# Performance work log

Measured on AMD Instinct MI355X. Metric: run time of the kernel, lower is better.

Reference implementation:

```python
import jax, jax.numpy as jnp
import numpy as np

HIDDEN = 512
IN_DIM = 512
N_ACT = 64
N_AGENTS = 8


def kalei_linear(x, ids, W, b, t):
    """x: [N, I]; ids: [N]; W: [O, I]; b: [O]; t: [A, O, I] -> [N, O].
    w_a = sign(W) * relu(|W| - sigmoid(t_a)); y_n = w_{ids[n]} @ x_n + b.
    """
    Wm = jnp.sign(W)[None] * jax.nn.relu(jnp.abs(W)[None] - jax.nn.sigmoid(t))  # [A,O,I]
    y = jnp.einsum('aoi,ni->nao', Wm, x)          # [N, A, O] batched masked GEMM
    y = jnp.take_along_axis(y, ids[:, None, None], axis=1)[:, 0]  # [N, O]
    return y + b[None, :]


def gru_cell(x, h, w_ih, w_hh, b_ih, b_hh):
    gi = x @ w_ih.T + b_ih
    gh = h @ w_hh.T + b_hh
    i_r, i_z, i_n = jnp.split(gi, 3, axis=-1)
    h_r, h_z, h_n = jnp.split(gh, 3, axis=-1)
    r = jax.nn.sigmoid(i_r + h_r)
    z = jax.nn.sigmoid(i_z + h_z)
    n = jnp.tanh(i_n + r * h_n)
    return (1.0 - z) * n + z * h


def setup_inputs() -> dict:
    key = jax.random.key(0)
    ks = jax.random.split(key, 20)
    B, A = 2048, N_AGENTS
    scale_init_lo, scale_init_hi = 3.0, 4.0  # -(rand*scale + bias) in [-4, -3]

    def thr(k, o, i):
        return -jax.random.uniform(k, (A, o, i), jnp.float32, scale_init_lo, scale_init_hi)

    w_scale = 0.05
    inp = {
        'inputs': jax.random.normal(ks[0], (B, A, IN_DIM), jnp.float32),
        'hidden_state': jax.random.normal(ks[1], (B, A, HIDDEN), jnp.float32),
        'agent_ids': jax.random.randint(ks[2], (B, A), 0, A),
        'fc1_w': jax.random.normal(ks[3], (HIDDEN, IN_DIM), jnp.float32) * w_scale,
        'fc1_b': jax.random.normal(ks[4], (HIDDEN,), jnp.float32) * w_scale,
        'fc1_t': thr(ks[5], HIDDEN, IN_DIM),
        'gru_wih': jax.random.normal(ks[6], (3 * HIDDEN, HIDDEN), jnp.float32) * w_scale,
        'gru_whh': jax.random.normal(ks[7], (3 * HIDDEN, HIDDEN), jnp.float32) * w_scale,
        'gru_bih': jax.random.normal(ks[8], (3 * HIDDEN,), jnp.float32) * w_scale,
        'gru_bhh': jax.random.normal(ks[9], (3 * HIDDEN,), jnp.float32) * w_scale,
        'fc2_w': jax.random.normal(ks[10], (HIDDEN, HIDDEN), jnp.float32) * w_scale,
        'fc2_b': jax.random.normal(ks[11], (HIDDEN,), jnp.float32) * w_scale,
        'fc2_t': thr(ks[12], HIDDEN, HIDDEN),
        'fc3_w': jax.random.normal(ks[13], (HIDDEN, HIDDEN), jnp.float32) * w_scale,
        'fc3_b': jax.random.normal(ks[14], (HIDDEN,), jnp.float32) * w_scale,
        'fc3_t': thr(ks[15], HIDDEN, HIDDEN),
        'fc4_w': jax.random.normal(ks[16], (N_ACT, HIDDEN), jnp.float32) * w_scale,
        'fc4_b': jax.random.normal(ks[17], (N_ACT,), jnp.float32) * w_scale,
        'fc4_t': thr(ks[18], N_ACT, HIDDEN),
    }
    return inp


def reference(inputs, hidden_state, agent_ids,
              fc1_w, fc1_b, fc1_t,
              gru_wih, gru_whh, gru_bih, gru_bhh,
              fc2_w, fc2_b, fc2_t,
              fc3_w, fc3_b, fc3_t,
              fc4_w, fc4_b, fc4_t):
    b, a, e = inputs.shape
    x = inputs.reshape(-1, e)                  # [N, e]
    ids = agent_ids.reshape(-1)                # [N]
    h_in = hidden_state.reshape(-1, HIDDEN)    # [N, H]

    x = jax.nn.relu(kalei_linear(x, ids, fc1_w, fc1_b, fc1_t))
    h = gru_cell(x, h_in, gru_wih, gru_whh, gru_bih, gru_bhh)
    q = jax.nn.relu(kalei_linear(h, ids, fc2_w, fc2_b, fc2_t))
    q = jax.nn.relu(kalei_linear(q, ids, fc3_w, fc3_b, fc3_t))
    q = kalei_linear(q, ids, fc4_w, fc4_b, fc4_t)
    return q.reshape(b, a, -1), h.reshape(b, a, -1)
```

## Files before the change

### kernel.cpp

```cpp
#include <hip/hip_runtime.h>
#include <hip/hip_bf16.h>
#include <stdint.h>

#define HID 512
#define NACT 64
#define NAG 8
#define NR 16384
#define BMT 128
#define MAXTILES 136

typedef __bf16 bf16_t;
typedef __bf16 bf16x4 __attribute__((ext_vector_type(4)));
typedef __bf16 bf16x8 __attribute__((ext_vector_type(8)));
typedef float  f32x16 __attribute__((ext_vector_type(16)));

#define MFMA32(a,b,c) __builtin_amdgcn_mfma_f32_32x32x16_bf16((a),(b),(c),0,0,0)

#define OFF_META 0
#define OFF_PERM 4096
#define OFF_WM1  (128*1024)
#define OFF_WM2  (OFF_WM1 + NAG*HID*HID*2)
#define OFF_WM3  (OFF_WM2 + NAG*HID*HID*2)
#define OFF_WM4  (OFF_WM3 + NAG*HID*HID*2)
#define OFF_WIH  (OFF_WM4 + NAG*NACT*HID*2)
#define OFF_WHH  (OFF_WIH + 3*HID*HID*2)
#define OFF_XS   (OFF_WHH + 3*HID*HID*2)
#define OFF_HS   (OFF_XS + (size_t)NR*HID*2)
#define OFF_B1   (OFF_HS + (size_t)NR*HID*2)

__device__ inline void load_lds16(const void* g, void* l) {
  __builtin_amdgcn_global_load_lds((__attribute__((address_space(1))) void*)g,
                                   (__attribute__((address_space(3))) void*)l,
                                   16, 0, 0);
}

template<int N> __device__ inline void wait_vmcnt() {
  asm volatile("s_waitcnt vmcnt(%0)" :: "n"(N) : "memory");
}
__device__ inline void wait_lgkm0() {
  asm volatile("s_waitcnt lgkmcnt(0)" ::: "memory");
}
#define BAR() __builtin_amdgcn_s_barrier()

__device__ inline bf16x8 lds_frag(const bf16_t* base, int r, int cb) {
  return *(const bf16x8*)((const char*)base + r*128 + ((cb*16) ^ ((r&7)<<4)));
}

__device__ inline void store8bf(void* dst, float4 a, float4 b) {
  union { bf16_t h[8]; uint4 u; } p;
  p.h[0]=(bf16_t)a.x; p.h[1]=(bf16_t)a.y; p.h[2]=(bf16_t)a.z; p.h[3]=(bf16_t)a.w;
  p.h[4]=(bf16_t)b.x; p.h[5]=(bf16_t)b.y; p.h[6]=(bf16_t)b.z; p.h[7]=(bf16_t)b.w;
  *(uint4*)dst = p.u;
}

__device__ inline float kmask(float w, float t) {
  float s = 1.f / (1.f + __expf(-t));
  float m = fabsf(w) - s;
  return m > 0.f ? copysignf(m, w) : 0.f;
}
__device__ inline float sigm(float x) { return 1.f / (1.f + __expf(-x)); }
__device__ inline float tanh_f(float x) {
  float e = __expf(2.f * fabsf(x));
  return copysignf(1.f - 2.f/(e + 1.f), x);
}

__global__ void k_prep(const float* __restrict__ f1w, const float* __restrict__ f1t,
                       const float* __restrict__ f2w, const float* __restrict__ f2t,
                       const float* __restrict__ f3w, const float* __restrict__ f3t,
                       const float* __restrict__ f4w, const float* __restrict__ f4t,
                       const float* __restrict__ gih, const float* __restrict__ ghh,
                       bf16_t* __restrict__ wm1, bf16_t* __restrict__ wm2,
                       bf16_t* __restrict__ wm3, bf16_t* __restrict__ wm4,
                       bf16_t* __restrict__ wihb, bf16_t* __restrict__ whhb,
                       int* __restrict__ meta)
{
  const int tid = threadIdx.x;
  if (blockIdx.x == 0 && tid < 32) meta[tid] = 0;
  long v = (long)blockIdx.x * 256 + tid;
  const long VR1 = 524288;
  if (v < 3*VR1) {
    int which = (int)(v / VR1);
    long e = (v - (long)which*VR1) * 4;
    const float* W = which==0 ? f1w : (which==1 ? f2w : f3w);
    const float* T = which==0 ? f1t : (which==1 ? f2t : f3t);
    bf16_t* O = which==0 ? wm1 : (which==1 ? wm2 : wm3);
    long oi = e & (long)(HID*HID - 1);
    float4 w = *(const float4*)(W + oi);
    float4 t = *(const float4*)(T + e);
    bf16x4 o;
    o[0]=(bf16_t)kmask(w.x,t.x); o[1]=(bf16_t)kmask(w.y,t.y);
    o[2]=(bf16_t)kmask(w.z,t.z); o[3]=(bf16_t)kmask(w.w,t.w);
    *(bf16x4*)(O + e) = o;
  } else if (v < 3*VR1 + 65536) {
    long e = (v - 3*VR1) * 4;
    long oi = e & (long)(NACT*HID - 1);
    float4 w = *(const float4*)(f4w + oi);
    float4 t = *(const float4*)(f4t + e);
    bf16x4 o;
    o[0]=(bf16_t)kmask(w.x,t.x); o[1]=(bf16_t)kmask(w.y,t.y);
    o[2]=(bf16_t)kmask(w.z,t.z); o[3]=(bf16_t)kmask(w.w,t.w);
    *(bf16x4*)(wm4 + e) = o;
  } else if (v < 3*VR1 + 65536 + 196608) {
    long e = (v - (3*VR1 + 65536)) * 4;
    float4 x = *(const float4*)(gih + e);
    bf16x4 o; o[0]=(bf16_t)x.x; o[1]=(bf16_t)x.y; o[2]=(bf16_t)x.z; o[3]=(bf16_t)x.w;
    *(bf16x4*)(wihb + e) = o;
  } else if (v < 3*VR1 + 65536 + 2*196608) {
    long e = (v - (3*VR1 + 65536 + 196608)) * 4;
    float4 x = *(const float4*)(ghh + e);
    bf16x4 o; o[0]=(bf16_t)x.x; o[1]=(bf16_t)x.y; o[2]=(bf16_t)x.z; o[3]=(bf16_t)x.w;
    *(bf16x4*)(whhb + e) = o;
  }
}

__global__ void k_count(const int* __restrict__ ids, int* __restrict__ meta) {
  int n = blockIdx.x*256 + threadIdx.x;
  atomicAdd(&meta[ids[n]], 1);
}

__global__ void k_td(int* __restrict__ meta) {
  int off = 0, nt = 0;
  for (int a = 0; a < NAG; ++a) {
    int c = meta[a];
    meta[8+a] = off;
    for (int t = 0; t*BMT < c; ++t) {
      meta[32 + nt]  = off + t*BMT;
      meta[192 + nt] = (c - t*BMT < BMT) ? (c - t*BMT) : BMT;
      meta[352 + nt] = a;
      ++nt;
    }
    off += c;
  }
  meta[16] = nt;
}

__global__ void k_scatter(const int* __restrict__ ids, int* __restrict__ meta,
                          int* __restrict__ perm) {
  int n = blockIdx.x*256 + threadIdx.x;
  int a = ids[n];
  int pos = atomicAdd(&meta[8+a], 1);
  perm[pos] = n;
}

__global__ void k_gather(const float* __restrict__ inputs, const float* __restrict__ hidden,
                         const int* __restrict__ perm,
                         bf16_t* __restrict__ xs, bf16_t* __restrict__ hs)
{
  int tid = threadIdx.x;
  int rb = blockIdx.x*4 + (tid>>6);
  int m = rb & (NR-1);
  int src = perm[m];
  const float* sp; bf16_t* op;
  if (rb < NR) { sp = inputs + (size_t)src*HID; op = xs + (size_t)m*HID; }
  else         { sp = hidden + (size_t)src*HID; op = hs + (size_t)m*HID; }
  int c = (tid&63)*8;
  float4 v0 = *(const float4*)(sp + c);
  float4 v1 = *(const float4*)(sp + c + 4);
  store8bf(op + c, v0, v1);
}

template<int BN, int OTOT, int OUTMODE>
__global__ __launch_bounds__(256)
void k_fc(const bf16_t* __restrict__ a_bf, const bf16_t* __restrict__ wbase,
          const float* __restrict__ bias,
          bf16_t* __restrict__ out_bf, float* __restrict__ out_f32,
          const int* __restrict__ meta, const int* __restrict__ perm)
{
  constexpr int FN  = BN/64;
  constexpr int NLB = BN/32;
  constexpr int NLD = 4 + NLB;
  const int bx = blockIdx.x;
  if (bx >= meta[16]) return;
  const int m0 = meta[32+bx], rows = meta[192+bx], agent = meta[352+bx];
  const int o0 = blockIdx.y * BN;
  const bf16_t* W = wbase + (size_t)agent * OTOT * HID;

  __shared__ bf16_t lds[2][(BMT + BN)*64];

  const int tid = threadIdx.x, lane = tid & 63, wid = tid >> 6;
  const int wrow = wid & 1, wcol = wid >> 1;
  const int gsw = (lane&7) ^ ((lane>>3)&7);

  f32x16 zero;
  #pragma unroll
  for (int i = 0; i < 16; ++i) zero[i] = 0.f;
  f32x16 acc[2][FN];
  #pragma unroll
  for (int i = 0; i < 2; ++i)
    #pragma unroll
    for (int j = 0; j < FN; ++j) acc[i][j] = zero;

  auto stage = [&](int kp, int s) {
    const int k0 = kp * 64;
    bf16_t* LA = &lds[s][0];
    bf16_t* LB = &lds[s][BMT*64];
    #pragma unroll
    for (int q = 0; q < 4; ++q) {
      int i = wid*4 + q;
      int r = i*8 + (lane>>3);
      int rl = r < rows ? r : rows-1;
      load_lds16(a_bf + (size_t)(m0+rl)*HID + k0 + gsw*8, (char*)LA + i*1024);
    }
    #pragma unroll
    for (int q = 0; q < NLB; ++q) {
      int i = wid*NLB + q;
      int r = i*8 + (lane>>3);
      load_lds16(W + (size_t)(o0+r)*HID + k0 + gsw*8, (char*)LB + i*1024);
    }
  };

  auto compute = [&](int s) {
    const bf16_t* LA = &lds[s][0];
    const bf16_t* LB = &lds[s][BMT*64];
    #pragma unroll
    for (int kk = 0; kk < 4; ++kk) {
      const int cbb = kk*2 + (lane>>5);
      bf16x8 af[2];
      #pragma unroll
      for (int fm = 0; fm < 2; ++fm)
        af[fm] = lds_frag(LA, wrow*64 + fm*32 + (lane&31), cbb);
      #pragma unroll
      for (int fn = 0; fn < FN; ++fn) {
        bf16x8 bv = lds_frag(LB, wcol*(BN/2) + fn*32 + (lane&31), cbb);
        #pragma unroll
        for (int fm = 0; fm < 2; ++fm)
          acc[fm][fn] = MFMA32(af[fm], bv, acc[fm][fn]);
      }
    }
  };

  stage(0, 0); stage(1, 1);
  for (int t = 0; t < 6; ++t) {
    wait_vmcnt<NLD>(); BAR();
    compute(t & 1);
    wait_lgkm0(); BAR();
    stage(t + 2, t & 1);
  }
  wait_vmcnt<NLD>(); BAR(); compute(0); wait_lgkm0(); BAR();
  wait_vmcnt<0>();   BAR(); compute(1);

  #pragma unroll
  for (int fn = 0; fn < FN; ++fn) {
    int col = o0 + wcol*(BN/2) + fn*32 + (lane&31);
    float bv = bias[col];
    #pragma unroll
    for (int fm = 0; fm < 2; ++fm) {
      #pragma unroll
      for (int g = 0; g < 16; ++g) {
        int rl = wrow*64 + fm*32 + 4*(lane>>5) + (g&3) + 8*(g>>2);
        if (rl < rows) {
          float y = acc[fm][fn][g] + bv;
          if constexpr (OUTMODE == 0) {
            y = fmaxf(y, 0.f);
            out_bf[(size_t)(m0+rl)*OTOT + col] = (bf16_t)y;
          } else {
            out_f32[(size_t)perm[m0+rl]*OTOT + col] = y;
          }
        }
      }
    }
  }
}

__global__ __launch_bounds__(256)
void k_gru(const bf16_t* __restrict__ x1, const bf16_t* __restrict__ hs,
           const float* __restrict__ hidden,
           const bf16_t* __restrict__ wih, const bf16_t* __restrict__ whh,
           const float* __restrict__ bih, const float* __restrict__ bhh,
           bf16_t* __restrict__ hbuf, float* __restrict__ hout,
           const int* __restrict__ perm)
{
  const int m0 = blockIdx.x * BMT;
  const int j0 = blockIdx.y * 64;
  const int tid = threadIdx.x, lane = tid & 63, wid = tid >> 6;
  const int wrow = wid & 1, wcol = wid >> 1;
  const int gsw = (lane&7) ^ ((lane>>3)&7);

  __shared__ bf16_t lds[2][(BMT + 192)*64];

  f32x16 zero;
  #pragma unroll
  for (int i = 0; i < 16; ++i) zero[i] = 0.f;
  f32x16 ar[2], az[2], an[2], ah[2];
  ar[0]=ar[1]=az[0]=az[1]=an[0]=an[1]=ah[0]=ah[1]=zero;

  auto stage = [&](int kp, int s) {
    const bf16_t* A  = (kp < 8) ? x1  : hs;
    const bf16_t* Wg = (kp < 8) ? wih : whh;
    const int k0 = (kp & 7) * 64;
    bf16_t* LA = &lds[s][0];
    bf16_t* LB = &lds[s][BMT*64];
    #pragma unroll
    for (int q = 0; q < 4; ++q) {
      int i = wid*4 + q;
      int r = i*8 + (lane>>3);
      load_lds16(A + (size_t)(m0+r)*HID + k0 + gsw*8, (char*)LA + i*1024);
    }
    #pragma unroll
    for (int q = 0; q < 6; ++q) {
      int i = wid*6 + q;
      int gate = i >> 3, rb = i & 7;
      int rr = gate*HID + j0 + rb*8 + (lane>>3);
      load_lds16(Wg + (size_t)rr*HID + k0 + gsw*8, (char*)LB + i*1024);
    }
  };

  auto compute = [&](int s, f32x16 (&a3)[2]) {
    const bf16_t* LA = &lds[s][0];
    const bf16_t* LB = &lds[s][BMT*64];
    #pragma unroll
    for (int kk = 0; kk < 4; ++kk) {
      const int cbb = kk*2 + (lane>>5);
      bf16x8 af0 = lds_frag(LA, wrow*64 +      (lane&31), cbb);
      bf16x8 af1 = lds_frag(LA, wrow*64 + 32 + (lane&31), cbb);
      const int rb = wcol*32 + (lane&31);
      bf16x8 b0 = lds_frag(LB,        rb, cbb);
      bf16x8 b1 = lds_frag(LB + 4096, rb, cbb);
      bf16x8 b2 = lds_frag(LB + 8192, rb, cbb);
      ar[0] = MFMA32(af0, b0, ar[0]); ar[1] = MFMA32(af1, b0, ar[1]);
      az[0] = MFMA32(af0, b1, az[0]); az[1] = MFMA32(af1, b1, az[1]);
      a3[0] = MFMA32(af0, b2, a3[0]); a3[1] = MFMA32(af1, b2, a3[1]);
    }
  };

  stage(0, 0); stage(1, 1);
  for (int t = 0; t < 8; ++t) {
    wait_vmcnt<10>(); BAR();
    compute(t & 1, an);
    wait_lgkm0(); BAR();
    stage(t + 2, t & 1);
  }
  for (int t = 8; t < 14; ++t) {
    wait_vmcnt<10>(); BAR();
    compute(t & 1, ah);
    wait_lgkm0(); BAR();
    stage(t + 2, t & 1);
  }
  wait_vmcnt<10>(); BAR(); compute(0, ah); wait_lgkm0(); BAR();
  wait_vmcnt<0>();  BAR(); compute(1, ah);

  const int col = j0 + wcol*32 + (lane&31);
  const float b_r  = bih[col]        + bhh[col];
  const float b_z  = bih[512 + col]  + bhh[512 + col];
  const float b_in = bih[1024 + col];
  const float b_hn = bhh[1024 + col];
  #pragma unroll
  for (int fm = 0; fm < 2; ++fm) {
    #pragma unroll
    for (int g = 0; g < 16; ++g) {
      int rl = wrow*64 + fm*32 + 4*(lane>>5) + (g&3) + 8*(g>>2);
      int m = m0 + rl;
      int src = perm[m];
      float hp = hidden[(size_t)src*HID + col];
      float rg = sigm(ar[fm][g] + b_r);
      float zg = sigm(az[fm][g] + b_z);
      float ng = tanh_f(an[fm][g] + b_in + rg*(ah[fm][g] + b_hn));
      float h  = (1.f - zg)*ng + zg*hp;
      hbuf[(size_t)m*HID + col] = (bf16_t)h;
      hout[(size_t)src*HID + col] = h;
    }
  }
}

extern "C" void kernel_launch(void* const* d_in, const int* in_sizes, int n_in,
                              void* d_out, int out_size, void* d_ws, size_t ws_size,
                              hipStream_t stream) {
  const float* inputs  = (const float*)d_in[0];
  const float* hidden  = (const float*)d_in[1];
  const int*   ids     = (const int*)  d_in[2];
  const float* fc1_w   = (const float*)d_in[3];
  const float* fc1_b   = (const float*)d_in[4];
  const float* fc1_t   = (const float*)d_in[5];
  const float* gru_wih = (const float*)d_in[6];
  const float* gru_whh = (const float*)d_in[7];
  const float* gru_bih = (const float*)d_in[8];
  const float* gru_bhh = (const float*)d_in[9];
  const float* fc2_w   = (const float*)d_in[10];
  const float* fc2_b   = (const float*)d_in[11];
  const float* fc2_t   = (const float*)d_in[12];
  const float* fc3_w   = (const float*)d_in[13];
  const float* fc3_b   = (const float*)d_in[14];
  const float* fc3_t   = (const float*)d_in[15];
  const float* fc4_w   = (const float*)d_in[16];
  const float* fc4_b   = (const float*)d_in[17];
  const float* fc4_t   = (const float*)d_in[18];

  char* ws = (char*)d_ws;
  int*    meta = (int*)   (ws + OFF_META);
  int*    perm = (int*)   (ws + OFF_PERM);
  bf16_t* wm1  = (bf16_t*)(ws + OFF_WM1);
  bf16_t* wm2  = (bf16_t*)(ws + OFF_WM2);
  bf16_t* wm3  = (bf16_t*)(ws + OFF_WM3);
  bf16_t* wm4  = (bf16_t*)(ws + OFF_WM4);
  bf16_t* wihb = (bf16_t*)(ws + OFF_WIH);
  bf16_t* whhb = (bf16_t*)(ws + OFF_WHH);
  bf16_t* xs   = (bf16_t*)(ws + OFF_XS);
  bf16_t* hs   = (bf16_t*)(ws + OFF_HS);
  bf16_t* b1   = (bf16_t*)(ws + OFF_B1);

  float* q_out = (float*)d_out;
  float* h_out = q_out + (size_t)NR * NACT;

  k_prep<<<7936, 256, 0, stream>>>(fc1_w, fc1_t, fc2_w, fc2_t, fc3_w, fc3_t,
                                   fc4_w, fc4_t, gru_wih, gru_whh,
                                   wm1, wm2, wm3, wm4, wihb, whhb, meta);
  k_count<<<64, 256, 0, stream>>>(ids, meta);
  k_td<<<1, 1, 0, stream>>>(meta);
  k_scatter<<<64, 256, 0, stream>>>(ids, meta, perm);
  k_gather<<<8192, 256, 0, stream>>>(inputs, hidden, perm, xs, hs);

  k_fc<128, HID, 0><<<dim3(MAXTILES, 4), 256, 0, stream>>>(
      xs, wm1, fc1_b, b1, nullptr, meta, perm);
  k_gru<<<dim3(NR/BMT, 8), 256, 0, stream>>>(b1, hs, hidden, wihb, whhb,
                                             gru_bih, gru_bhh, xs, h_out, perm);
  k_fc<128, HID, 0><<<dim3(MAXTILES, 4), 256, 0, stream>>>(
      xs, wm2, fc2_b, b1, nullptr, meta, perm);
  k_fc<128, HID, 0><<<dim3(MAXTILES, 4), 256, 0, stream>>>(
      b1, wm3, fc3_b, hs, nullptr, meta, perm);
  k_fc<64, NACT, 1><<<dim3(MAXTILES, 1), 256, 0, stream>>>(
      hs, wm4, fc4_b, nullptr, q_out, meta, perm);
}
```

Before: 330.2 us.

## Interleave next-tile global loads with MFMA sub-steps and raise occupancy hint

Replaces the two-stage prefetch pipeline in the FC and GRU GEMM kernels with a schedule that issues the next K-tile's global-to-LDS loads in four slices, one between each MFMA sub-step. Each sub-step reads its fragments, barriers, then runs its MFMAs at raised wave priority. Launch bounds now request two blocks per CU. This aims to hide load latency behind compute and add occupancy, but it makes the prefetch distance one tile instead of two and adds barriers per sub-step, which may expose memory latency.

```diff
diff --git a/kernel.cpp b/kernel.cpp
--- a/kernel.cpp
+++ b/kernel.cpp
@@ -160,7 +160,7 @@
 }
 
 template<int BN, int OTOT, int OUTMODE>
-__global__ __launch_bounds__(256)
+__global__ __launch_bounds__(256, 2)
 void k_fc(const bf16_t* __restrict__ a_bf, const bf16_t* __restrict__ wbase,
           const float* __restrict__ bias,
           bf16_t* __restrict__ out_bf, float* __restrict__ out_f32,
@@ -180,6 +180,7 @@
   const int tid = threadIdx.x, lane = tid & 63, wid = tid >> 6;
   const int wrow = wid & 1, wcol = wid >> 1;
   const int gsw = (lane&7) ^ ((lane>>3)&7);
+  const int lr8 = lane >> 3;
 
   f32x16 zero;
   #pragma unroll
@@ -190,54 +191,55 @@
     #pragma unroll
     for (int j = 0; j < FN; ++j) acc[i][j] = zero;
 
-  auto stage = [&](int kp, int s) {
+  auto stage_part = [&](int kp, int s, int lo, int hi) {
+    if (kp >= 8) return;
     const int k0 = kp * 64;
     bf16_t* LA = &lds[s][0];
     bf16_t* LB = &lds[s][BMT*64];
     #pragma unroll
-    for (int q = 0; q < 4; ++q) {
-      int i = wid*4 + q;
-      int r = i*8 + (lane>>3);
-      int rl = r < rows ? r : rows-1;
-      load_lds16(a_bf + (size_t)(m0+rl)*HID + k0 + gsw*8, (char*)LA + i*1024);
-    }
-    #pragma unroll
-    for (int q = 0; q < NLB; ++q) {
-      int i = wid*NLB + q;
-      int r = i*8 + (lane>>3);
-      load_lds16(W + (size_t)(o0+r)*HID + k0 + gsw*8, (char*)LB + i*1024);
+    for (int i = 0; i < NLD; ++i) {
+      if (i < lo || i >= hi) continue;
+      if (i < 4) {
+        int c = wid*4 + i;
+        int r = c*8 + lr8;
+        int rl = r < rows ? r : rows-1;
+        load_lds16(a_bf + (size_t)(m0+rl)*HID + k0 + gsw*8, (char*)LA + c*1024);
+      } else {
+        int c = wid*NLB + (i-4);
+        int r = c*8 + lr8;
+        load_lds16(W + (size_t)(o0+r)*HID + k0 + gsw*8, (char*)LB + c*1024);
+      }
     }
   };
 
-  auto compute = [&](int s) {
-    const bf16_t* LA = &lds[s][0];
-    const bf16_t* LB = &lds[s][BMT*64];
+  stage_part(0, 0, 0, NLD);
+  for (int t = 0; t < 8; ++t) {
+    wait_vmcnt<0>(); BAR();
+    const bf16_t* LA = &lds[t&1][0];
+    const bf16_t* LB = &lds[t&1][BMT*64];
     #pragma unroll
     for (int kk = 0; kk < 4; ++kk) {
       const int cbb = kk*2 + (lane>>5);
-      bf16x8 af[2];
+      bf16x8 af[2], bf[FN];
       #pragma unroll
       for (int fm = 0; fm < 2; ++fm)
         af[fm] = lds_frag(LA, wrow*64 + fm*32 + (lane&31), cbb);
       #pragma unroll
-      for (int fn = 0; fn < FN; ++fn) {
-        bf16x8 bv = lds_frag(LB, wcol*(BN/2) + fn*32 + (lane&31), cbb);
+      for (int fn = 0; fn < FN; ++fn)
+        bf[fn] = lds_frag(LB, wcol*(BN/2) + fn*32 + (lane&31), cbb);
+      stage_part(t+1, (t+1)&1, kk*NLD/4, (kk+1)*NLD/4);
+      BAR();
+      wait_lgkm0();
+      __builtin_amdgcn_s_setprio(1);
+      #pragma unroll
+      for (int fn = 0; fn < FN; ++fn)
         #pragma unroll
         for (int fm = 0; fm < 2; ++fm)
-          acc[fm][fn] = MFMA32(af[fm], bv, acc[fm][fn]);
-      }
-    }
-  };
-
-  stage(0, 0); stage(1, 1);
-  for (int t = 0; t < 6; ++t) {
-    wait_vmcnt<NLD>(); BAR();
-    compute(t & 1);
-    wait_lgkm0(); BAR();
-    stage(t + 2, t & 1);
+          acc[fm][fn] = MFMA32(af[fm], bf[fn], acc[fm][fn]);
+      __builtin_amdgcn_s_setprio(0);
+      BAR();
+    }
   }
-  wait_vmcnt<NLD>(); BAR(); compute(0); wait_lgkm0(); BAR();
-  wait_vmcnt<0>();   BAR(); compute(1);
 
   #pragma unroll
   for (int fn = 0; fn < FN; ++fn) {
@@ -262,7 +264,7 @@
   }
 }
 
-__global__ __launch_bounds__(256)
+__global__ __launch_bounds__(256, 2)
 void k_gru(const bf16_t* __restrict__ x1, const bf16_t* __restrict__ hs,
            const float* __restrict__ hidden,
            const bf16_t* __restrict__ wih, const bf16_t* __restrict__ whh,
@@ -275,6 +277,7 @@
   const int tid = threadIdx.x, lane = tid & 63, wid = tid >> 6;
   const int wrow = wid & 1, wcol = wid >> 1;
   const int gsw = (lane&7) ^ ((lane>>3)&7);
+  const int lr8 = lane >> 3;
 
   __shared__ bf16_t lds[2][(BMT + 192)*64];
 
@@ -284,30 +287,33 @@
   f32x16 ar[2], az[2], an[2], ah[2];
   ar[0]=ar[1]=az[0]=az[1]=an[0]=an[1]=ah[0]=ah[1]=zero;
 
-  auto stage = [&](int kp, int s) {
+  auto stage_part = [&](int kp, int s, int lo, int hi) {
+    if (kp >= 16) return;
     const bf16_t* A  = (kp < 8) ? x1  : hs;
     const bf16_t* Wg = (kp < 8) ? wih : whh;
     const int k0 = (kp & 7) * 64;
     bf16_t* LA = &lds[s][0];
     bf16_t* LB = &lds[s][BMT*64];
     #pragma unroll
-    for (int q = 0; q < 4; ++q) {
-      int i = wid*4 + q;
-      int r = i*8 + (lane>>3);
-      load_lds16(A + (size_t)(m0+r)*HID + k0 + gsw*8, (char*)LA + i*1024);
-    }
-    #pragma unroll
-    for (int q = 0; q < 6; ++q) {
-      int i = wid*6 + q;
-      int gate = i >> 3, rb = i & 7;
-      int rr = gate*HID + j0 + rb*8 + (lane>>3);
-      load_lds16(Wg + (size_t)rr*HID + k0 + gsw*8, (char*)LB + i*1024);
+    for (int i = 0; i < 10; ++i) {
+      if (i < lo || i >= hi) continue;
+      if (i < 4) {
+        int c = wid*4 + i;
+        int r = c*8 + lr8;
+        load_lds16(A + (size_t)(m0+r)*HID + k0 + gsw*8, (char*)LA + c*1024);
+      } else {
+        int c = wid*6 + (i-4);
+        int r = c*8 + lr8;
+        int wr = (r>>6)*HID + j0 + (r&63);
+        load_lds16(Wg + (size_t)wr*HID + k0 + gsw*8, (char*)LB + c*1024);
+      }
     }
   };
 
-  auto compute = [&](int s, f32x16 (&a3)[2]) {
-    const bf16_t* LA = &lds[s][0];
-    const bf16_t* LB = &lds[s][BMT*64];
+  auto step = [&](int t, f32x16 (&a3)[2]) {
+    wait_vmcnt<0>(); BAR();
+    const bf16_t* LA = &lds[t&1][0];
+    const bf16_t* LB = &lds[t&1][BMT*64];
     #pragma unroll
     for (int kk = 0; kk < 4; ++kk) {
       const int cbb = kk*2 + (lane>>5);
@@ -317,27 +323,21 @@
       bf16x8 b0 = lds_frag(LB,        rb, cbb);
       bf16x8 b1 = lds_frag(LB + 4096, rb, cbb);
       bf16x8 b2 = lds_frag(LB + 8192, rb, cbb);
+      stage_part(t+1, (t+1)&1, kk*10/4, (kk+1)*10/4);
+      BAR();
+      wait_lgkm0();
+      __builtin_amdgcn_s_setprio(1);
       ar[0] = MFMA32(af0, b0, ar[0]); ar[1] = MFMA32(af1, b0, ar[1]);
       az[0] = MFMA32(af0, b1, az[0]); az[1] = MFMA32(af1, b1, az[1]);
       a3[0] = MFMA32(af0, b2, a3[0]); a3[1] = MFMA32(af1, b2, a3[1]);
+      __builtin_amdgcn_s_setprio(0);
+      BAR();
     }
   };
 
-  stage(0, 0); stage(1, 1);
-  for (int t = 0; t < 8; ++t) {
-    wait_vmcnt<10>(); BAR();
-    compute(t & 1, an);
-    wait_lgkm0(); BAR();
-    stage(t + 2, t & 1);
-  }
-  for (int t = 8; t < 14; ++t) {
-    wait_vmcnt<10>(); BAR();
-    compute(t & 1, ah);
-    wait_lgkm0(); BAR();
-    stage(t + 2, t & 1);
-  }
-  wait_vmcnt<10>(); BAR(); compute(0, ah); wait_lgkm0(); BAR();
-  wait_vmcnt<0>();  BAR(); compute(1, ah);
+  stage_part(0, 0, 0, 10);
+  for (int t = 0; t < 8; ++t)  step(t, an);
+  for (int t = 8; t < 16; ++t) step(t, ah);
 
   const int col = j0 + wcol*32 + (lane&31);
   const float b_r  = bih[col]        + bhh[col];
```

After: 331.1 us. About the same (+0.3%).
